# Optimization experiments

Hardware: AMD Instinct MI355X
Metric: run time of the kernel (lower is better)

The kernel has to match this reference:

```python
import jax, jax.numpy as jnp
import numpy as np

B, CIN, COUT, H, W = 1, 2, 2, 180, 360
E, NL, LM, MM, HID = 256, 4, 90, 91, 512  # embed, layers, lmax, mmax, mlp hidden
RB = W // 2 + 1  # rfft bins = 181


def setup_inputs() -> dict:
    key = jax.random.key(0)
    ks = jax.random.split(key, 14)
    s = 0.02
    return {
        "x": jax.random.normal(ks[0], (B, CIN, H, W), jnp.float32),
        "enc_w1": jax.random.normal(ks[1], (E, CIN), jnp.float32) * s,
        "enc_w2": jax.random.normal(ks[2], (E, E), jnp.float32) * s,
        "pos": jax.random.normal(ks[3], (1, E, H, W), jnp.float32) * s,
        "leg_fwd": jax.random.normal(ks[4], (MM, LM, H), jnp.float32) / np.float32(np.sqrt(H)),
        "leg_inv": jax.random.normal(ks[5], (MM, LM, H), jnp.float32) / np.float32(np.sqrt(LM)),
        "w_spec_r": jax.random.normal(ks[6], (NL, E, E, LM), jnp.float32) * s,
        "w_spec_i": jax.random.normal(ks[7], (NL, E, E, LM), jnp.float32) * s,
        "w_inner": jax.random.normal(ks[8], (NL, E, E), jnp.float32) * s,
        "w_mlp1": jax.random.normal(ks[9], (NL, HID, E), jnp.float32) * s,
        "w_mlp2": jax.random.normal(ks[10], (NL, E, HID), jnp.float32) * s,
        "dec_w1": jax.random.normal(ks[11], (E, E + CIN), jnp.float32) * s,
        "dec_w2": jax.random.normal(ks[12], (COUT, E), jnp.float32) * s,
    }


def _conv1x1(w, x):
    # w: [O, C], x: [B, C, H, W]
    return jnp.einsum("oc,bchw->bohw", w, x)


def _sht(x, leg_fwd):
    # forward spherical-harmonic transform: rfft over lon + Legendre over lat
    xf = jnp.fft.rfft(x, axis=-1)[..., :MM]            # [B, C, H, MM] complex64
    return jnp.einsum("bchm,mlh->bclm", xf, leg_fwd)   # [B, C, LM, MM]


def _isht(c, leg_inv):
    xf = jnp.einsum("bclm,mlh->bchm", c, leg_inv)      # [B, C, H, MM]
    xf = jnp.pad(xf, ((0, 0), (0, 0), (0, 0), (0, RB - MM)))
    return jnp.fft.irfft(xf, n=W, axis=-1)             # [B, C, H, W] real


def _gelu(x):
    return jax.nn.gelu(x, approximate=False)


def reference(x, enc_w1, enc_w2, pos, leg_fwd, leg_inv, w_spec_r, w_spec_i,
              w_inner, w_mlp1, w_mlp2, dec_w1, dec_w2):
    inp = x
    # encoder (pointwise MLP) + direct positional embedding
    h = _gelu(_conv1x1(enc_w1, inp))
    h = _conv1x1(enc_w2, h) + pos
    # FNO blocks: identity norms, dhconv spectral filter, linear inner skip,
    # MLP, identity outer skip (act_layer0 never applied per source bug)
    for i in range(NL):
        residual = h
        coeff = _sht(h, leg_fwd)
        w = w_spec_r[i] + 1j * w_spec_i[i]                  # [E, E, LM]
        coeff = jnp.einsum("bclm,ocl->bolm", coeff, w)
        h = _isht(coeff, leg_inv)
        h = h + _conv1x1(w_inner[i], residual)
        h = _conv1x1(w_mlp2[i], _gelu(_conv1x1(w_mlp1[i], h)))
        h = h + residual
    # big skip: concat raw input channels, then pointwise decoder
    h = jnp.concatenate([h, inp], axis=1)
    h = _gelu(_conv1x1(dec_w1, h))
    return _conv1x1(dec_w2, h)
```

## Files before the change

kernel.cpp:

```cpp
#include <hip/hip_runtime.h>
#include <hip/hip_bf16.h>
#include <math.h>
#include <stdio.h>

typedef long long ll;
typedef __bf16 bf16x8 __attribute__((ext_vector_type(8)));
typedef float f32x4 __attribute__((ext_vector_type(4)));

#define CIN    2
#define COUTC  2
#define Hh     180
#define Ww     360
#define Ech    256
#define NLAYERS 4
#define LMAX   90
#define MMAX   91
#define HIDD   512
#define NPIX   (Hh*Ww)
#define CHROWS (Ech*Hh)
#define S2     (2*MMAX)
#define CDIV(a,b) (((a)+(b)-1)/(b))

struct GemmBP {
    const __hip_bfloat16* A; const __hip_bfloat16* B;
    const float* Dd; void* C;
    ll sAb; int ldA;
    ll sBb; int ldB;
    ll sCb, sCi, sCj;
    ll sDb, sDi, sDj;
    int M, N, K;
    int epi;
};

__device__ __forceinline__ void glds16(const __hip_bfloat16* g, __hip_bfloat16* l) {
    __builtin_amdgcn_global_load_lds(
        (const __attribute__((address_space(1))) unsigned int*)g,
        (__attribute__((address_space(3))) unsigned int*)l,
        16, 0, 0);
}

__global__ __launch_bounds__(256)
void gemm_bf(GemmBP p) {
    __shared__ __hip_bfloat16 As[4096];
    __shared__ __hip_bfloat16 Bs[4096];
    const int t = threadIdx.x;
    const int lane = t & 63, wv = t >> 6;
    const int wr = wv >> 1, wc = wv & 1;
    const int z = blockIdx.z;
    const int i0 = blockIdx.y * 128, j0 = blockIdx.x * 128;
    const __hip_bfloat16* Ab = p.A + (ll)z * p.sAb;
    const __hip_bfloat16* Bb = p.B + (ll)z * p.sBb;

    f32x4 acc[4][4] = {};

    const bool isB = (wv >= 2);
    const int kgbase = (wv & 1) * 2;
    const __hip_bfloat16* Gp = isB ? Bb : Ab;
    const int ld  = isB ? p.ldB : p.ldA;
    const int lim = isB ? p.N : p.M;
    const int rb0 = isB ? j0 : i0;
    __hip_bfloat16* Ls = isB ? Bs : As;

    for (int kt = 0; kt < p.K; kt += 32) {
        __syncthreads();
#pragma unroll
        for (int s = 0; s < 4; ++s) {
            int kg = kgbase + (s >> 1), half = s & 1;
            int r = half * 64 + lane;
            int grow = rb0 + r;
            __hip_bfloat16* ldst = Ls + kg * 1024 + half * 512;
            const __hip_bfloat16* gsrc = Gp + (ll)grow * ld + kt + kg * 8;
            if (grow < lim) glds16(gsrc, ldst);
        }
        __syncthreads();

        bf16x8 af[4], bg[4];
#pragma unroll
        for (int f = 0; f < 4; ++f) {
            af[f] = *(const bf16x8*)(As + (lane >> 4) * 1024 + (wr * 64 + f * 16 + (lane & 15)) * 8);
            bg[f] = *(const bf16x8*)(Bs + (lane >> 4) * 1024 + (wc * 64 + f * 16 + (lane & 15)) * 8);
        }
#pragma unroll
        for (int fr = 0; fr < 4; ++fr)
#pragma unroll
            for (int fn = 0; fn < 4; ++fn)
                acc[fr][fn] = __builtin_amdgcn_mfma_f32_16x16x32_bf16(af[fr], bg[fn], acc[fr][fn], 0, 0, 0);
    }

    float* Cf = (float*)p.C;
    __hip_bfloat16* Ch = (__hip_bfloat16*)p.C;
    const float* Db = p.Dd ? (p.Dd + (ll)z * p.sDb) : nullptr;
    const ll cb = (ll)z * p.sCb;
#pragma unroll
    for (int fr = 0; fr < 4; ++fr) {
#pragma unroll
        for (int j = 0; j < 4; ++j) {
            int row = i0 + wr * 64 + fr * 16 + (lane >> 4) * 4 + j;
            if (row >= p.M) continue;
#pragma unroll
            for (int fn = 0; fn < 4; ++fn) {
                int col = j0 + wc * 64 + fn * 16 + (lane & 15);
                if (col >= p.N) continue;
                float r = acc[fr][fn][j];
                if (p.epi & 1) r += Db[(ll)row * p.sDi + (ll)col * p.sDj];
                if (p.epi & 2) r = 0.5f * r * (1.0f + erff(r * 0.70710678118654752f));
                ll ca = cb + (ll)row * p.sCi + (ll)col * p.sCj;
                if (p.epi & 4) Ch[ca] = __hip_bfloat16(r);
                else           Cf[ca] = r;
            }
        }
    }
}

struct GemmP {
    const float* A; const float* Bm; const float* Dd; float* C;
    ll sAb, sAi, sAk;
    ll sBb, sBk, sBj;
    ll sCb, sCi, sCj;
    ll sDb, sDi, sDj;
    int M, N, K;
    float alpha;
    int epi;
};

#define BM 64
#define BN 64
#define BK 16

__global__ __launch_bounds__(256)
void gemm_f32(GemmP p) {
    __shared__ float As[BM][BK];
    __shared__ float Bs[BK][BN];
    const int t  = threadIdx.x;
    const int tx = t & 15, ty = t >> 4;
    const int z  = blockIdx.z;
    const int i0 = blockIdx.y * BM;
    const int j0 = blockIdx.x * BN;
    const float* Ab = p.A  + (ll)z * p.sAb;
    const float* Bb = p.Bm + (ll)z * p.sBb;
    float acc[4][4] = {};
    for (int kt = 0; kt < p.K; kt += BK) {
#pragma unroll
        for (int s = 0; s < 4; ++s) {
            int idx = t + 256 * s;
            int i = idx >> 4, k = idx & 15;
            int gi = i0 + i, gk = kt + k;
            As[i][k] = (gi < p.M && gk < p.K) ? Ab[(ll)gi * p.sAi + (ll)gk * p.sAk] : 0.0f;
        }
#pragma unroll
        for (int s = 0; s < 4; ++s) {
            int idx = t + 256 * s;
            int k = idx >> 6, j = idx & 63;
            int gk = kt + k, gj = j0 + j;
            Bs[k][j] = (gk < p.K && gj < p.N) ? Bb[(ll)gk * p.sBk + (ll)gj * p.sBj] : 0.0f;
        }
        __syncthreads();
#pragma unroll
        for (int kk = 0; kk < BK; ++kk) {
            float a[4], b[4];
#pragma unroll
            for (int ii = 0; ii < 4; ++ii) a[ii] = As[ty + 16*ii][kk];
#pragma unroll
            for (int jj = 0; jj < 4; ++jj) b[jj] = Bs[kk][tx + 16*jj];
#pragma unroll
            for (int ii = 0; ii < 4; ++ii)
#pragma unroll
                for (int jj = 0; jj < 4; ++jj)
                    acc[ii][jj] += a[ii] * b[jj];
        }
        __syncthreads();
    }
    float* Cb = p.C + (ll)z * p.sCb;
    const float* Db = p.Dd ? (p.Dd + (ll)z * p.sDb) : nullptr;
#pragma unroll
    for (int ii = 0; ii < 4; ++ii) {
        int gi = i0 + ty + 16*ii;
        if (gi >= p.M) continue;
#pragma unroll
        for (int jj = 0; jj < 4; ++jj) {
            int gj = j0 + tx + 16*jj;
            if (gj >= p.N) continue;
            float r = p.alpha * acc[ii][jj];
            if (p.epi & 1) r += Db[(ll)gi * p.sDi + (ll)gj * p.sDj];
            if (p.epi & 2) r = 0.5f * r * (1.0f + erff(r * 0.70710678118654752f));
            Cb[(ll)gi * p.sCi + (ll)gj * p.sCj] = r;
        }
    }
}

__global__ __launch_bounds__(256)
void transp_cv(const float* __restrict__ src, __hip_bfloat16* __restrict__ dst, int R, int C,
               ll srcB, ll srcR, ll dstB, ll dstR, float sign) {
    __shared__ float tile[32][33];
    ll b = blockIdx.z;
    int r0 = blockIdx.y * 32, c0 = blockIdx.x * 32;
    const float* s = src + b * srcB;
    __hip_bfloat16* d = dst + b * dstB;
    int tx = threadIdx.x, ty = threadIdx.y;
    for (int k = 0; k < 32; k += 8) {
        int r = r0 + ty + k, c = c0 + tx;
        if (r < R && c < C) tile[ty + k][tx] = s[(ll)r * srcR + c];
    }
    __syncthreads();
    for (int k = 0; k < 32; k += 8) {
        int c = c0 + ty + k, r = r0 + tx;
        if (r < R && c < C) d[(ll)c * dstR + r] = __hip_bfloat16(sign * tile[tx][ty + k]);
    }
}

__global__ void conv_pad(const float* __restrict__ src, __hip_bfloat16* __restrict__ dst,
                         int R, int Cu, int Cp) {
    ll idx = (ll)blockIdx.x * blockDim.x + threadIdx.x;
    if (idx >= (ll)R * Cp) return;
    int r = (int)(idx / Cp), c = (int)(idx % Cp);
    dst[idx] = (c < Cu) ? __hip_bfloat16(src[(ll)r * Cu + c]) : __hip_bfloat16(0.0f);
}

__global__ void conv_mat(const float* __restrict__ src, __hip_bfloat16* __restrict__ dst,
                         int R, int C, int srcLd) {
    ll idx = (ll)blockIdx.x * blockDim.x + threadIdx.x;
    if (idx >= (ll)R * C) return;
    int r = (int)(idx / C), c = (int)(idx % C);
    dst[idx] = __hip_bfloat16(src[(ll)r * srcLd + c]);
}

__global__ void zero_pad(__hip_bfloat16* __restrict__ dst, ll rows, int ld, int c0, int c1) {
    ll idx = (ll)blockIdx.x * blockDim.x + threadIdx.x;
    int w = c1 - c0;
    if (idx >= rows * w) return;
    ll r = idx / w; int c = c0 + (int)(idx % w);
    dst[r * ld + c] = __hip_bfloat16(0.0f);
}

__global__ void build_dmt(__hip_bfloat16* __restrict__ DmT) {
    int idx = blockIdx.x * blockDim.x + threadIdx.x;
    if (idx >= S2 * 384) return;
    int s = idx / 384, w = idx % 384;
    float v = 0.0f;
    if (w < Ww) {
        int m = s % MMAX;
        float ang = (2.0f * (float)M_PI / (float)Ww) * (float)((w * m) % Ww);
        v = (s < MMAX) ? cosf(ang) : -sinf(ang);
    }
    DmT[idx] = __hip_bfloat16(v);
}

__global__ void build_dinvt(__hip_bfloat16* __restrict__ DinvT) {
    int idx = blockIdx.x * blockDim.x + threadIdx.x;
    if (idx >= Ww * 192) return;
    int w = idx / 192, s = idx % 192;
    float v = 0.0f;
    if (s < S2) {
        int m = s % MMAX;
        float ang = (2.0f * (float)M_PI / (float)Ww) * (float)((w * m) % Ww);
        float scale = (m == 0) ? (1.0f / (float)Ww) : (2.0f / (float)Ww);
        if (s < MMAX) v = scale * cosf(ang);
        else          v = (m == 0) ? 0.0f : -scale * sinf(ang);
    }
    DinvT[idx] = __hip_bfloat16(v);
}

__global__ void build_lf(const float* __restrict__ leg_fwd, __hip_bfloat16* __restrict__ LF) {
    int idx = blockIdx.x * blockDim.x + threadIdx.x;
    if (idx >= S2 * LMAX * 192) return;
    int s = idx / (LMAX * 192);
    int rem = idx % (LMAX * 192);
    int l = rem / 192, h = rem % 192;
    float v = (h < Hh) ? leg_fwd[(ll)(s % MMAX) * LMAX * Hh + (ll)l * Hh + h] : 0.0f;
    LF[idx] = __hip_bfloat16(v);
}

__global__ void build_lit(const float* __restrict__ leg_inv, __hip_bfloat16* __restrict__ LIT) {
    int idx = blockIdx.x * blockDim.x + threadIdx.x;
    if (idx >= MMAX * Hh * 96) return;
    int m = idx / (Hh * 96);
    int rem = idx % (Hh * 96);
    int h = rem / 96, l = rem % 96;
    float v = (l < LMAX) ? leg_inv[(ll)m * LMAX * Hh + (ll)l * Hh + h] : 0.0f;
    LIT[idx] = __hip_bfloat16(v);
}

static inline void gemmb(hipStream_t st, const __hip_bfloat16* A, int ldA, ll sAb,
                         const __hip_bfloat16* B, int ldB, ll sBb,
                         void* C, ll sCb, ll sCi, ll sCj,
                         const float* Dd, ll sDb, ll sDi, ll sDj,
                         int M, int N, int K, int nb, int epi) {
    GemmBP p{A, B, Dd, C, sAb, ldA, sBb, ldB, sCb, sCi, sCj, sDb, sDi, sDj, M, N, K, epi};
    dim3 g(CDIV(N, 128), CDIV(M, 128), nb);
    gemm_bf<<<g, dim3(256), 0, st>>>(p);
}

static inline void gemm(hipStream_t st, const float* A, const float* B, float* C, const float* Add,
                        int M, int N, int K, int nb,
                        ll sAb, ll sAi, ll sAk,
                        ll sBb, ll sBk, ll sBj,
                        ll sCb, ll sCi, ll sCj,
                        ll sDb, ll sDi, ll sDj,
                        float alpha, int epi) {
    GemmP p{A, B, Add, C, sAb, sAi, sAk, sBb, sBk, sBj, sCb, sCi, sCj, sDb, sDi, sDj,
            M, N, K, alpha, epi};
    dim3 g(CDIV(N, BN), CDIV(M, BM), nb);
    gemm_f32<<<g, dim3(256), 0, st>>>(p);
}

static inline void tcv(hipStream_t st, const float* src, __hip_bfloat16* dst, int R, int C,
                       ll srcB, ll srcR, ll dstB, ll dstR, int nb, float sign) {
    dim3 g(CDIV(C, 32), CDIV(R, 32), nb);
    transp_cv<<<g, dim3(32, 8), 0, st>>>(src, dst, R, C, srcB, srcR, dstB, dstR, sign);
}

extern "C" void kernel_launch(void* const* d_in, const int* in_sizes, int n_in,
                              void* d_out, int out_size, void* d_ws, size_t ws_size,
                              hipStream_t stream) {
    const float* x        = (const float*)d_in[0];
    const float* enc_w1   = (const float*)d_in[1];
    const float* enc_w2   = (const float*)d_in[2];
    const float* pos      = (const float*)d_in[3];
    const float* leg_fwd  = (const float*)d_in[4];
    const float* leg_inv  = (const float*)d_in[5];
    const float* w_spec_r = (const float*)d_in[6];
    const float* w_spec_i = (const float*)d_in[7];
    const float* w_inner  = (const float*)d_in[8];
    const float* w_mlp1   = (const float*)d_in[9];
    const float* w_mlp2   = (const float*)d_in[10];
    const float* dec_w1   = (const float*)d_in[11];
    const float* dec_w2   = (const float*)d_in[12];
    float* out = (float*)d_out;
    float* wsp = (float*)d_ws;

    float* pool = wsp;
    __hip_bfloat16* HCB  = (__hip_bfloat16*)(pool + 0);
    float*          XF   = pool + 8847360;
    __hip_bfloat16* XT   = (__hip_bfloat16*)(pool + 0);
    float*          CF   = pool + 8847360;
    __hip_bfloat16* TCF  = (__hip_bfloat16*)(pool + 4472832);
    __hip_bfloat16* WC   = (__hip_bfloat16*)(pool + 13040640);
    float*          CO   = pool + 0;
    __hip_bfloat16* COT  = (__hip_bfloat16*)(pool + 8847360);
    float*          YT   = pool + 0;
    __hip_bfloat16* YF   = (__hip_bfloat16*)(pool + 8847360);
    float*          VF   = pool + 13271040;
    __hip_bfloat16* HPB  = (__hip_bfloat16*)(pool + 0);
    __hip_bfloat16* V2PB = (__hip_bfloat16*)(pool + 0);
    __hip_bfloat16* GT   = (__hip_bfloat16*)(pool + 8294400);
    float*          V1   = pool + 0;
    __hip_bfloat16* V1PB = (__hip_bfloat16*)(pool + 16588800);
    const ll POOLSZ = 29859840;

    ll off = POOLSZ;
    float* HC  = wsp + off; off += 16588800;
    float* HC2 = wsp + off; off += 16588800;
    __hip_bfloat16* DmT   = (__hip_bfloat16*)(wsp + off); off += 34944;
    __hip_bfloat16* DinvT = (__hip_bfloat16*)(wsp + off); off += 34560;
    __hip_bfloat16* LF    = (__hip_bfloat16*)(wsp + off); off += 1572480;
    __hip_bfloat16* LIT   = (__hip_bfloat16*)(wsp + off); off += 786240;
    __hip_bfloat16* ENC2B = (__hip_bfloat16*)(wsp + off); off += 32768;
    __hip_bfloat16* WINB  = (__hip_bfloat16*)(wsp + off); off += 32768;
    __hip_bfloat16* WM1B  = (__hip_bfloat16*)(wsp + off); off += 65536;
    __hip_bfloat16* WM2B  = (__hip_bfloat16*)(wsp + off); off += 65536;
    __hip_bfloat16* DW1B  = (__hip_bfloat16*)(wsp + off); off += 32768;
    __hip_bfloat16* DW2B  = (__hip_bfloat16*)(wsp + off); off += 256;

    if ((size_t)(off * 4) > ws_size) {
        fprintf(stderr, "kernel_launch: ws too small: need %lld bytes, have %zu\n",
                off * 4, ws_size);
        return;
    }

    const ll EE = (ll)Ech * Ech;

    build_dmt  <<<CDIV(S2 * 384, 256), 256, 0, stream>>>(DmT);
    build_dinvt<<<CDIV(Ww * 192, 256), 256, 0, stream>>>(DinvT);
    build_lf   <<<CDIV(S2 * LMAX * 192, 256), 256, 0, stream>>>(leg_fwd, LF);
    build_lit  <<<CDIV(MMAX * Hh * 96, 256), 256, 0, stream>>>(leg_inv, LIT);
    conv_mat<<<CDIV(256 * 256, 256), 256, 0, stream>>>(enc_w2, ENC2B, 256, 256, 256);
    conv_mat<<<CDIV(256 * 256, 256), 256, 0, stream>>>(dec_w1, DW1B, 256, 256, Ech + CIN);
    conv_mat<<<CDIV(2 * 256, 256), 256, 0, stream>>>(dec_w2, DW2B, 2, 256, 256);

    gemm(stream, enc_w1, x, V1, nullptr, Ech, NPIX, CIN, 1,
         0, CIN, 1,  0, NPIX, 1,  0, NPIX, 1,  0, 0, 0,  1.0f, 2);
    tcv(stream, V1, V1PB, 256, NPIX, 0, NPIX, 0, 256, 1, 1.0f);
    gemmb(stream, ENC2B, 256, 0, V1PB, 256, 0, HC, 0, NPIX, 1,
          pos, 0, NPIX, 1, 256, NPIX, 256, 1, 1);

    float* curH = HC;
    float* curN = HC2;

    for (int l = 0; l < NLAYERS; ++l) {
        const float* wr_l = w_spec_r + (ll)l * EE * LMAX;
        const float* wi_l = w_spec_i + (ll)l * EE * LMAX;

        conv_mat<<<CDIV(256 * 256, 256), 256, 0, stream>>>(w_inner + (ll)l * EE, WINB, 256, 256, 256);
        conv_mat<<<CDIV(512 * 256, 256), 256, 0, stream>>>(w_mlp1 + (ll)l * HIDD * Ech, WM1B, 512, 256, 256);
        conv_mat<<<CDIV(256 * 512, 256), 256, 0, stream>>>(w_mlp2 + (ll)l * Ech * HIDD, WM2B, 256, 512, 512);

        conv_pad<<<CDIV(46080LL * 384, 256), 256, 0, stream>>>(curH, HCB, CHROWS, Ww, 384);
        gemmb(stream, HCB, 384, 0, DmT, 384, 0, XF, 0, 182, 1,
              nullptr, 0, 0, 0, CHROWS, S2, 384, 1, 0);
        zero_pad<<<CDIV(46592LL * 12, 256), 256, 0, stream>>>(XT, 46592LL, 192, 180, 192);
        tcv(stream, XF, XT, Hh, S2, (ll)Hh * S2, S2, 192, 49152, 256, 1.0f);
        gemmb(stream, XT, 192, 49152, LF, 192, 17280, CF, 23040, 90, 1,
              nullptr, 0, 0, 0, 256, LMAX, 192, 182, 0);
        for (int pp = 0; pp < 2; ++pp)
            tcv(stream, CF + (ll)pp * 2096640, TCF + (ll)pp * 256, 256, LMAX,
                23040, LMAX, 512, 46592, MMAX, 1.0f);
        tcv(stream, wr_l, WC,                256, LMAX, 23040, LMAX, 512, 262144, 256,  1.0f);
        tcv(stream, wi_l, WC + 256,          256, LMAX, 23040, LMAX, 512, 262144, 256, -1.0f);
        tcv(stream, wi_l, WC + 131072,       256, LMAX, 23040, LMAX, 512, 262144, 256,  1.0f);
        tcv(stream, wr_l, WC + 131072 + 256, 256, LMAX, 23040, LMAX, 512, 262144, 256,  1.0f);
        gemmb(stream, WC, 512, 262144, TCF, 512, 46592, CO, 46592, 91, 1,
              nullptr, 0, 0, 0, 512, MMAX, 512, LMAX, 0);
        zero_pad<<<CDIV(46592LL * 6, 256), 256, 0, stream>>>(COT, 46592LL, 96, 90, 96);
        tcv(stream, CO, COT, LMAX, MMAX, 91, 46592, 96, 49152, 512, 1.0f);
        gemmb(stream, COT, 96, 49152, LIT, 96, 17280, YT, 92160, 180, 1,
              nullptr, 0, 0, 0, 512, Hh, 96, MMAX, 0);
        zero_pad<<<CDIV(46080LL * 10, 256), 256, 0, stream>>>(YF, 46080LL, 192, 182, 192);
        for (int pp = 0; pp < 2; ++pp)
            tcv(stream, YT + (ll)pp * 46080, YF + (ll)pp * 91, MMAX, CHROWS,
                0, 92160, 0, 192, 1, 1.0f);
        gemmb(stream, YF, 192, 0, DinvT, 192, 0, VF, 0, 360, 1,
              nullptr, 0, 0, 0, CHROWS, Ww, 192, 1, 0);
        tcv(stream, curH, HPB, 256, NPIX, 0, NPIX, 0, 256, 1, 1.0f);
        gemmb(stream, WINB, 256, 0, HPB, 256, 0, VF, 0, NPIX, 1,
              VF, 0, NPIX, 1, 256, NPIX, 256, 1, 1);
        tcv(stream, VF, V2PB, 256, NPIX, 0, NPIX, 0, 256, 1, 1.0f);
        gemmb(stream, V2PB, 256, 0, WM1B, 256, 0, GT, 0, 512, 1,
              nullptr, 0, 0, 0, NPIX, HIDD, 256, 1, 6);
        gemmb(stream, WM2B, 512, 0, GT, 512, 0, curN, 0, NPIX, 1,
              curH, 0, NPIX, 1, 256, NPIX, 512, 1, 1);

        float* tmp = curH; curH = curN; curN = tmp;
    }

    __hip_bfloat16* HPBd = (__hip_bfloat16*)(pool + 0);
    float* T2 = VF;
    tcv(stream, curH, HPBd, 256, NPIX, 0, NPIX, 0, 256, 1, 1.0f);
    gemmb(stream, DW1B, 256, 0, HPBd, 256, 0, T2, 0, NPIX, 1,
          nullptr, 0, 0, 0, 256, NPIX, 256, 1, 0);
    gemm(stream, dec_w1 + Ech, x, T2, T2, Ech, NPIX, CIN, 1,
         0, Ech + CIN, 1,  0, NPIX, 1,  0, NPIX, 1,  0, NPIX, 1,  1.0f, 3);
    __hip_bfloat16* T2PB = (__hip_bfloat16*)(pool + 0);
    tcv(stream, T2, T2PB, 256, NPIX, 0, NPIX, 0, 256, 1, 1.0f);
    gemmb(stream, T2PB, 256, 0, DW2B, 256, 0, out, 0, 1, NPIX,
          nullptr, 0, 0, 0, NPIX, COUTC, 256, 1, 0);
}
```

Measured before the change: 2.861 ms.

## Double-buffer LDS tiles in bf16 GEMM to overlap global loads with MFMA

The GEMM kernel now keeps two LDS buffers for the A and B tiles. It issues the asynchronous global-to-LDS loads for the next K-slice before running the MFMAs on the current one, and drops one of the two barriers per iteration. Per-thread global pointers and bounds checks are also computed once before the loop instead of every iteration. This is meant to hide global load latency behind compute, at the cost of doubling LDS use to 32KB per block, which may reduce occupancy. Correctness relies on the single barrier per iteration being enough to order the async LDS writes.

```diff
diff --git a/kernel.cpp b/kernel.cpp
--- a/kernel.cpp
+++ b/kernel.cpp
@@ -41,51 +41,66 @@
 
 __global__ __launch_bounds__(256)
 void gemm_bf(GemmBP p) {
-    __shared__ __hip_bfloat16 As[4096];
-    __shared__ __hip_bfloat16 Bs[4096];
+    __shared__ __hip_bfloat16 As[2][4096];
+    __shared__ __hip_bfloat16 Bs[2][4096];
     const int t = threadIdx.x;
     const int lane = t & 63, wv = t >> 6;
     const int wr = wv >> 1, wc = wv & 1;
     const int z = blockIdx.z;
     const int i0 = blockIdx.y * 128, j0 = blockIdx.x * 128;
-    const __hip_bfloat16* Ab = p.A + (ll)z * p.sAb;
-    const __hip_bfloat16* Bb = p.B + (ll)z * p.sBb;
-
-    f32x4 acc[4][4] = {};
 
     const bool isB = (wv >= 2);
     const int kgbase = (wv & 1) * 2;
-    const __hip_bfloat16* Gp = isB ? Bb : Ab;
+    const __hip_bfloat16* Gp = isB ? (p.B + (ll)z * p.sBb) : (p.A + (ll)z * p.sAb);
     const int ld  = isB ? p.ldB : p.ldA;
     const int lim = isB ? p.N : p.M;
     const int rb0 = isB ? j0 : i0;
-    __hip_bfloat16* Ls = isB ? Bs : As;
-
-    for (int kt = 0; kt < p.K; kt += 32) {
-        __syncthreads();
-#pragma unroll
-        for (int s = 0; s < 4; ++s) {
-            int kg = kgbase + (s >> 1), half = s & 1;
-            int r = half * 64 + lane;
-            int grow = rb0 + r;
-            __hip_bfloat16* ldst = Ls + kg * 1024 + half * 512;
-            const __hip_bfloat16* gsrc = Gp + (ll)grow * ld + kt + kg * 8;
-            if (grow < lim) glds16(gsrc, ldst);
-        }
-        __syncthreads();
-
+
+    const __hip_bfloat16* gptr[4];
+    int ldoff[4];
+    bool ok[4];
+#pragma unroll
+    for (int s = 0; s < 4; ++s) {
+        int kg = kgbase + (s >> 1), half = s & 1;
+        int grow = rb0 + half * 64 + lane;
+        gptr[s] = Gp + (ll)grow * ld + kg * 8;
+        ldoff[s] = kg * 1024 + half * 512;
+        ok[s] = (grow < lim);
+    }
+
+    f32x4 acc[4][4] = {};
+
+    auto stage = [&](int buf, int kt) {
+        __hip_bfloat16* Ls = (isB ? Bs[buf] : As[buf]);
+#pragma unroll
+        for (int s = 0; s < 4; ++s)
+            if (ok[s]) glds16(gptr[s] + kt, Ls + ldoff[s]);
+    };
+    auto compute = [&](int buf) {
         bf16x8 af[4], bg[4];
 #pragma unroll
         for (int f = 0; f < 4; ++f) {
-            af[f] = *(const bf16x8*)(As + (lane >> 4) * 1024 + (wr * 64 + f * 16 + (lane & 15)) * 8);
-            bg[f] = *(const bf16x8*)(Bs + (lane >> 4) * 1024 + (wc * 64 + f * 16 + (lane & 15)) * 8);
+            af[f] = *(const bf16x8*)(As[buf] + (lane >> 4) * 1024 + (wr * 64 + f * 16 + (lane & 15)) * 8);
+            bg[f] = *(const bf16x8*)(Bs[buf] + (lane >> 4) * 1024 + (wc * 64 + f * 16 + (lane & 15)) * 8);
         }
 #pragma unroll
         for (int fr = 0; fr < 4; ++fr)
 #pragma unroll
             for (int fn = 0; fn < 4; ++fn)
                 acc[fr][fn] = __builtin_amdgcn_mfma_f32_16x16x32_bf16(af[fr], bg[fn], acc[fr][fn], 0, 0, 0);
-    }
+    };
+
+    stage(0, 0);
+    __syncthreads();
+
+    int cur = 0;
+    for (int kt = 32; kt < p.K; kt += 32) {
+        stage(cur ^ 1, kt);
+        compute(cur);
+        __syncthreads();
+        cur ^= 1;
+    }
+    compute(cur);
 
     float* Cf = (float*)p.C;
     __hip_bfloat16* Ch = (__hip_bfloat16*)p.C;
```

After: 2.878 ms. About the same (+0.6%).
